# Performance work log

Measured on AMD Instinct MI355X. Metric: run time of the kernel, lower is better.

The kernel has to match this reference:

```python
import jax, jax.numpy as jnp
import numpy as np

B, S, D = 2, 2048, 2048
HQ, HKV = 16, 4
HD = D // HQ  # 128


def setup_inputs() -> dict:
    key = jax.random.key(0)
    ks = jax.random.split(key, 8)
    init = lambda k, sh: jax.random.normal(k, sh, dtype=jnp.float32) * 0.02
    return {
        "q": jax.random.normal(ks[0], (B, S, D), dtype=jnp.float32),
        "kv": jax.random.normal(ks[1], (B, S, D), dtype=jnp.float32),
        "attn_bias": jax.random.normal(ks[2], (1, HQ, 1, S), dtype=jnp.float32),
        "attention_mask": jnp.ones((B, S), dtype=bool),
        "Wq_w": init(ks[3], (D, D)), "Wq_b": jnp.zeros((D,), jnp.float32),
        "Wk_w": init(ks[4], (HKV * HD, D)), "Wk_b": jnp.zeros((HKV * HD,), jnp.float32),
        "Wv_w": init(ks[5], (HKV * HD, D)), "Wv_b": jnp.zeros((HKV * HD,), jnp.float32),
        "Wo_w": init(ks[6], (D, D)), "Wo_b": jnp.zeros((D,), jnp.float32),
    }


def reference(q, kv, attn_bias, attention_mask, Wq_w, Wq_b, Wk_w, Wk_b, Wv_w, Wv_b, Wo_w, Wo_b):
    # Projections (torch nn.Linear: y = x @ W.T + b)
    query = q @ Wq_w.T + Wq_b        # [B,S,D]
    key_ = kv @ Wk_w.T + Wk_b        # [B,S,HKV*HD]
    value = kv @ Wv_w.T + Wv_b       # [B,S,HKV*HD]

    qh = query.reshape(B, S, HQ, HD).transpose(0, 2, 1, 3)   # [B,HQ,S,HD]
    kh = key_.reshape(B, S, HKV, HD).transpose(0, 2, 1, 3)   # [B,HKV,S,HD]
    vh = value.reshape(B, S, HKV, HD).transpose(0, 2, 1, 3)

    # GQA repeat_kv == torch.repeat_interleave along head dim
    n_rep = HQ // HKV
    kh = jnp.repeat(kh, n_rep, axis=1)  # [B,HQ,S,HD]
    vh = jnp.repeat(vh, n_rep, axis=1)

    scale = 1.0 / np.sqrt(HD).astype(np.float32)
    scores = jnp.einsum('bhqd,bhkd->bhqk', qh, kh) * scale  # [B,HQ,S,S]
    scores = scores + attn_bias  # broadcast [1,HQ,1,S]

    min_val = jnp.finfo(scores.dtype).min
    # key padding mask (True = keep)
    scores = jnp.where(attention_mask[:, None, None, :], scores, min_val)
    # causal mask
    causal = jnp.tril(jnp.ones((S, S), dtype=bool))
    scores = jnp.where(causal[None, None, :, :], scores, min_val)

    attn = jax.nn.softmax(scores, axis=-1)
    out = jnp.einsum('bhqk,bhkd->bhqd', attn, vh)           # [B,HQ,S,HD]
    out = out.transpose(0, 2, 1, 3).reshape(B, S, D)
    return out @ Wo_w.T + Wo_b
```

## Files before the change

kernel.cpp:

```cpp
#include <hip/hip_runtime.h>

typedef __bf16 bf16_t;
typedef __bf16 bf16x8 __attribute__((ext_vector_type(8)));
typedef float  f32x4  __attribute__((ext_vector_type(4)));

#define B_SZ    2
#define S_LEN   2048
#define D_MODEL 2048
#define HQ_     16
#define HD_     128
#define KV_D    512

typedef __attribute__((address_space(1))) const unsigned int gas_u32;
typedef __attribute__((address_space(3))) unsigned int las_u32;
__device__ __forceinline__ void glds16(const void* g, void* l) {
    __builtin_amdgcn_global_load_lds((gas_u32*)g, (las_u32*)l, 16, 0, 0);
}

template<int CTRL>
__device__ __forceinline__ float dppf(float x) {
    return __builtin_bit_cast(float,
        __builtin_amdgcn_update_dpp(0, __builtin_bit_cast(int, x), CTRL, 0xF, 0xF, false));
}
__device__ __forceinline__ float redmax16(float x) {
    x = fmaxf(x, dppf<0xB1>(x));
    x = fmaxf(x, dppf<0x4E>(x));
    x = fmaxf(x, dppf<0x141>(x));
    x = fmaxf(x, dppf<0x140>(x));
    return x;
}
__device__ __forceinline__ float redsum16(float x) {
    x += dppf<0xB1>(x);
    x += dppf<0x4E>(x);
    x += dppf<0x141>(x);
    x += dppf<0x140>(x);
    return x;
}

#define CB0 2097152u
#define CB1 4194304u
#define CB2 5242880u
#define CB3 5505024u
#define CB4 5767168u
#define CB5 6815744u
__global__ __launch_bounds__(256) void cast_all(const float* s0, const float* s1, const float* s2,
                                                const float* s3, const float* s4, const float* s5,
                                                bf16_t* d0, bf16_t* d1, bf16_t* d2,
                                                bf16_t* d3, bf16_t* d4, bf16_t* d5) {
    unsigned g = blockIdx.x * 256 + threadIdx.x;
    const float* src; bf16_t* dst; unsigned off;
    if (g < CB2) {
        if (g < CB0)      { src = s0; dst = d0; off = 0; }
        else if (g < CB1) { src = s1; dst = d1; off = CB0; }
        else              { src = s2; dst = d2; off = CB1; }
    } else {
        if (g < CB3)      { src = s3; dst = d3; off = CB2; }
        else if (g < CB4) { src = s4; dst = d4; off = CB3; }
        else              { src = s5; dst = d5; off = CB4; }
    }
    unsigned i = g - off;
    float4 v = ((const float4*)src)[i];
    bf16_t tmp[4] = {(bf16_t)v.x, (bf16_t)v.y, (bf16_t)v.z, (bf16_t)v.w};
    ((ushort4*)dst)[i] = *(ushort4*)tmp;
}

template<bool OUT_BF16>
__device__ __forceinline__ void gemm_nt_body(bf16_t* As, bf16_t* Bs,
                                             const bf16_t* __restrict__ A,
                                             const bf16_t* __restrict__ Bm,
                                             const float* __restrict__ bias,
                                             void* __restrict__ C,
                                             int M, int N, int K, int bx, int by) {
    const int tid  = threadIdx.x;
    const int lane = tid & 63;
    const int w    = tid >> 6;
    const int l16  = lane & 15;
    const int quad = lane >> 4;
    const int m0   = by * 128;
    const int n0   = bx * 128;
    const int moff = (w & 1) * 64;
    const int noff = (w >> 1) * 64;

    const int srow = w * 32 + (lane >> 2);
    const int scol = ((lane & 3) ^ ((lane >> 3) & 3)) * 8;
    const bf16_t* Ar = A  + (size_t)(m0 + srow) * K + scol;
    const bf16_t* Br = Bm + (size_t)(n0 + srow) * K + scol;
    bf16_t* asw = As + w * 1024;
    bf16_t* bsw = Bs + w * 1024;

    f32x4 acc[4][4];
    for (int i = 0; i < 4; ++i)
        for (int j = 0; j < 4; ++j) acc[i][j] = (f32x4){0.f, 0.f, 0.f, 0.f};

    const int nkt = K >> 5;
    for (int kt = 0; kt < nkt; ++kt) {
        const int ko = kt * 32;
        __syncthreads();
        glds16(Ar + ko,                  asw);
        glds16(Ar + (size_t)16 * K + ko, asw + 512);
        glds16(Br + ko,                  bsw);
        glds16(Br + (size_t)16 * K + ko, bsw + 512);
        __syncthreads();

        bf16x8 af[4], bfr[4];
        for (int i = 0; i < 4; ++i) {
            int row = moff + i * 16 + l16;
            af[i] = *(const bf16x8*)&As[row * 32 + ((quad ^ (row >> 1)) & 3) * 8];
        }
        for (int j = 0; j < 4; ++j) {
            int row = noff + j * 16 + l16;
            bfr[j] = *(const bf16x8*)&Bs[row * 32 + ((quad ^ (row >> 1)) & 3) * 8];
        }
        for (int i = 0; i < 4; ++i)
            for (int j = 0; j < 4; ++j)
                acc[i][j] = __builtin_amdgcn_mfma_f32_16x16x32_bf16(af[i], bfr[j], acc[i][j], 0, 0, 0);
    }

    for (int i = 0; i < 4; ++i) {
        int row = m0 + moff + i * 16 + quad * 4;
        for (int j = 0; j < 4; ++j) {
            int col = n0 + noff + j * 16 + l16;
            float bv = bias[col];
            for (int r = 0; r < 4; ++r) {
                float v = acc[i][j][r] + bv;
                if (OUT_BF16) ((bf16_t*)C)[(size_t)(row + r) * N + col] = (bf16_t)v;
                else          ((float*)C)[(size_t)(row + r) * N + col] = v;
            }
        }
    }
}

template<bool OUT_BF16>
__global__ __launch_bounds__(256) void gemm_nt_bias(const bf16_t* __restrict__ A,
                                                    const bf16_t* __restrict__ Bm,
                                                    const float* __restrict__ bias,
                                                    void* __restrict__ C,
                                                    int M, int N, int K) {
    __shared__ bf16_t As[128 * 32];
    __shared__ bf16_t Bs[128 * 32];
    gemm_nt_body<OUT_BF16>(As, Bs, A, Bm, bias, C, M, N, K, blockIdx.x, blockIdx.y);
}

__global__ __launch_bounds__(256) void gemm_nt_bias_kv(const bf16_t* __restrict__ A,
                                                       const bf16_t* __restrict__ Bk,
                                                       const bf16_t* __restrict__ Bv,
                                                       const float* __restrict__ bk,
                                                       const float* __restrict__ bv,
                                                       bf16_t* __restrict__ Ck,
                                                       bf16_t* __restrict__ Cv,
                                                       int M, int N, int K) {
    __shared__ bf16_t As[128 * 32];
    __shared__ bf16_t Bs[128 * 32];
    if (blockIdx.z == 0)
        gemm_nt_body<true>(As, Bs, A, Bk, bk, Ck, M, N, K, blockIdx.x, blockIdx.y);
    else
        gemm_nt_body<true>(As, Bs, A, Bv, bv, Cv, M, N, K, blockIdx.x, blockIdx.y);
}

__global__ __launch_bounds__(256) void transpose_v(const bf16_t* __restrict__ src,
                                                   bf16_t* __restrict__ dst) {
    __shared__ bf16_t T[64 * 72];
    const int t  = threadIdx.x;
    const int s0 = blockIdx.x * 64, c0 = blockIdx.y * 64, b = blockIdx.z;
    const int r = t >> 3, c8 = (t & 7) * 8;
    const bf16_t* sp = src + ((size_t)b * S_LEN + s0) * KV_D + c0;
    for (int i = 0; i < 64; i += 32) {
        int s = r + i;
        *(uint4*)&T[s * 72 + (c8 ^ (((s >> 3) & 7) * 8))] =
            *(const uint4*)&sp[(size_t)s * KV_D + c8];
    }
    __syncthreads();
    const int dr = t >> 3, s8 = (t & 7) * 8;
    bf16_t* dp = dst + ((size_t)b * KV_D + c0) * S_LEN + s0;
    for (int i = 0; i < 64; i += 32) {
        int d = dr + i;
        bf16_t tmp[8];
        for (int j = 0; j < 8; ++j) {
            int s = s8 + j;
            tmp[j] = T[s * 72 + (((d & ~7) ^ (((s >> 3) & 7) * 8)) | (d & 7))];
        }
        *(uint4*)&dp[(size_t)d * S_LEN + s8] = *(uint4*)tmp;
    }
}

__device__ __forceinline__ int ks_addr(int r, int c) {
    int ch = c >> 3;
    return r * 128 + ((ch & 8) | ((ch ^ r) & 7)) * 8 + (c & 7);
}
__device__ __forceinline__ int vt_addr(int d, int k) {
    return d * 64 + (((k >> 3) ^ d) & 7) * 8 + (k & 7);
}
__device__ __forceinline__ int ps_addr(int row, int c) {
    int ph = (row ^ (row >> 1)) & 7;
    return row * 64 + (((c >> 3) ^ ph) & 7) * 8 + (c & 7);
}

struct Strip {
    float m[4];
    float l[4];
    f32x4 o[8];
};

__device__ __forceinline__ void score_softmax(f32x4* s, Strip& st, bool diag,
                                              int qbase, int k0, const float* Bls,
                                              bf16_t* psw, int l16, int quad) {
    const float SCL2E = 0.08838834764831845f * 1.44269504088896f;
    float rowmax[4];
    for (int r = 0; r < 4; ++r) rowmax[r] = -__builtin_inff();
    for (int n = 0; n < 4; ++n) {
        int kc = k0 + n * 16 + l16;
        float bv = Bls[kc];
        for (int r = 0; r < 4; ++r) {
            float v = fmaf(s[n][r], SCL2E, bv);
            if (diag && kc > qbase + quad * 4 + r) v = -__builtin_inff();
            s[n][r] = v;
            rowmax[r] = fmaxf(rowmax[r], v);
        }
    }
    float alpha[4], rowsum[4];
    for (int r = 0; r < 4; ++r) {
        float mx = redmax16(rowmax[r]);
        float mnew = fmaxf(st.m[r], mx);
        alpha[r] = exp2f(st.m[r] - mnew);
        st.m[r] = mnew;
        rowsum[r] = 0.f;
    }
    for (int n = 0; n < 4; ++n)
        for (int r = 0; r < 4; ++r) {
            float pv = exp2f(s[n][r] - st.m[r]);
            psw[ps_addr(quad * 4 + r, n * 16 + l16)] = (bf16_t)pv;
            rowsum[r] += pv;
        }
    for (int r = 0; r < 4; ++r) {
        rowsum[r] = redsum16(rowsum[r]);
        st.l[r] = st.l[r] * alpha[r] + rowsum[r];
    }
    for (int d = 0; d < 8; ++d)
        for (int r = 0; r < 4; ++r) st.o[d][r] *= alpha[r];
}

__global__ __launch_bounds__(256, 2) void flash_attn(const bf16_t* __restrict__ Qg,
                                                     const bf16_t* __restrict__ Kg,
                                                     const bf16_t* __restrict__ Vt,
                                                     const float* __restrict__ bias,
                                                     bf16_t* __restrict__ Og) {
    const int p   = blockIdx.x;
    const int h   = blockIdx.y;
    const int b   = blockIdx.z;
    const int qtL = p, qtH = 31 - p;
    const int q0L = qtL * 64, q0H = qtH * 64;
    const int kvh = h >> 2;

    __shared__ bf16_t Ks[64 * 128];
    __shared__ bf16_t Vts[128 * 64];
    __shared__ bf16_t Ps[4 * 2 * 1024];
    __shared__ float  Bls[S_LEN];

    const int tid  = threadIdx.x;
    const int lane = tid & 63;
    const int w    = tid >> 6;
    const int l16  = lane & 15;
    const int quad = lane >> 4;
    const float L2E = 1.44269504088896f;

    for (int i = 0; i < 2; ++i) {
        int idx = tid + i * 256;
        float4 v = ((const float4*)(bias + h * S_LEN))[idx];
        ((float4*)Bls)[idx] = make_float4(v.x * L2E, v.y * L2E, v.z * L2E, v.w * L2E);
    }

    const bf16_t* qrowL = Qg + (size_t)(b * S_LEN + q0L + w * 16 + l16) * D_MODEL + h * HD_;
    const bf16_t* qrowH = Qg + (size_t)(b * S_LEN + q0H + w * 16 + l16) * D_MODEL + h * HD_;
    bf16x8 qfL[4], qfH[4];
    for (int d = 0; d < 4; ++d) {
        qfL[d] = *(const bf16x8*)&qrowL[d * 32 + quad * 8];
        qfH[d] = *(const bf16x8*)&qrowH[d * 32 + quad * 8];
    }

    const int kr  = tid >> 2;
    const int kc4 = (tid & 3) * 4;
    const int vd  = tid >> 1;
    const int vc4 = (tid & 1) * 4;
    const bf16_t* kbase = Kg + (size_t)(b * S_LEN) * KV_D + kvh * HD_;
    const bf16_t* vbase = Vt + ((size_t)(b * 4 + kvh) * HD_ + vd) * S_LEN;
    uint4 kpre[4], vpre[4];
    auto prefetch = [&](int k0) {
        const bf16_t* kp = kbase + (size_t)(k0 + kr) * KV_D;
        for (int i = 0; i < 4; ++i) kpre[i] = *(const uint4*)&kp[(kc4 + i) * 8];
        const bf16_t* vp = vbase + k0;
        for (int i = 0; i < 4; ++i) vpre[i] = *(const uint4*)&vp[(vc4 + i) * 8];
    };
    prefetch(0);

    Strip sL, sH;
    for (int r = 0; r < 4; ++r) {
        sL.m[r] = -__builtin_inff(); sL.l[r] = 0.f;
        sH.m[r] = -__builtin_inff(); sH.l[r] = 0.f;
    }
    for (int d = 0; d < 8; ++d) {
        sL.o[d] = (f32x4){0.f, 0.f, 0.f, 0.f};
        sH.o[d] = (f32x4){0.f, 0.f, 0.f, 0.f};
    }

    bf16_t* pswH = &Ps[w * 2048];
    bf16_t* pswL = pswH + 1024;

    for (int kt = 0; kt <= qtH; ++kt) {
        const int k0 = kt * 64;
        __syncthreads();
        for (int i = 0; i < 4; ++i) *(uint4*)&Ks[ks_addr(kr, (kc4 + i) * 8)] = kpre[i];
        for (int i = 0; i < 4; ++i) *(uint4*)&Vts[vt_addr(vd, (vc4 + i) * 8)] = vpre[i];
        __syncthreads();
        if (kt < qtH) prefetch(k0 + 64);

        const bool doL = (kt <= qtL);

        f32x4 accH[4], accL[4];
        for (int n = 0; n < 4; ++n) {
            accH[n] = (f32x4){0.f, 0.f, 0.f, 0.f};
            accL[n] = (f32x4){0.f, 0.f, 0.f, 0.f};
        }
        for (int dstep = 0; dstep < 4; ++dstep)
            for (int n = 0; n < 4; ++n) {
                bf16x8 bb = *(const bf16x8*)&Ks[ks_addr(n * 16 + l16, dstep * 32 + quad * 8)];
                accH[n] = __builtin_amdgcn_mfma_f32_16x16x32_bf16(qfH[dstep], bb, accH[n], 0, 0, 0);
                if (doL)
                    accL[n] = __builtin_amdgcn_mfma_f32_16x16x32_bf16(qfL[dstep], bb, accL[n], 0, 0, 0);
            }

        score_softmax(accH, sH, kt == qtH, q0H + w * 16, k0, Bls, pswH, l16, quad);
        if (doL) score_softmax(accL, sL, kt == qtL, q0L + w * 16, k0, Bls, pswL, l16, quad);

        for (int kstep = 0; kstep < 2; ++kstep) {
            bf16x8 aH = *(const bf16x8*)&pswH[ps_addr(l16, kstep * 32 + quad * 8)];
            bf16x8 aL;
            if (doL) aL = *(const bf16x8*)&pswL[ps_addr(l16, kstep * 32 + quad * 8)];
            for (int d = 0; d < 8; ++d) {
                bf16x8 bb = *(const bf16x8*)&Vts[vt_addr(d * 16 + l16, kstep * 32 + quad * 8)];
                sH.o[d] = __builtin_amdgcn_mfma_f32_16x16x32_bf16(aH, bb, sH.o[d], 0, 0, 0);
                if (doL)
                    sL.o[d] = __builtin_amdgcn_mfma_f32_16x16x32_bf16(aL, bb, sL.o[d], 0, 0, 0);
            }
        }
    }

    auto write_out = [&](Strip& st, int q0) {
        bf16_t* dst = Og + (size_t)(b * S_LEN + q0 + w * 16) * D_MODEL + h * HD_;
        float inv[4];
        for (int r = 0; r < 4; ++r) inv[r] = __builtin_amdgcn_rcpf(st.l[r]);
        for (int d = 0; d < 8; ++d)
            for (int r = 0; r < 4; ++r) {
                float v = st.o[d][r] * inv[r];
                dst[(size_t)(quad * 4 + r) * D_MODEL + d * 16 + l16] = (bf16_t)v;
            }
    };
    write_out(sH, q0H);
    write_out(sL, q0L);
}

extern "C" void kernel_launch(void* const* d_in, const int* in_sizes, int n_in,
                              void* d_out, int out_size, void* d_ws, size_t ws_size,
                              hipStream_t stream) {
    const float* q         = (const float*)d_in[0];
    const float* kv        = (const float*)d_in[1];
    const float* attn_bias = (const float*)d_in[2];
    const float* Wq_w = (const float*)d_in[4];
    const float* Wq_b = (const float*)d_in[5];
    const float* Wk_w = (const float*)d_in[6];
    const float* Wk_b = (const float*)d_in[7];
    const float* Wv_w = (const float*)d_in[8];
    const float* Wv_b = (const float*)d_in[9];
    const float* Wo_w = (const float*)d_in[10];
    const float* Wo_b = (const float*)d_in[11];
    float* out = (float*)d_out;

    const size_t MROWS = (size_t)B_SZ * S_LEN;
    char* ws = (char*)d_ws;
    size_t off = 0;
    auto alloc = [&](size_t elems) { bf16_t* p = (bf16_t*)(ws + off); off += elems * sizeof(bf16_t); return p; };
    bf16_t* qb     = alloc(MROWS * D_MODEL);
    bf16_t* kvb    = alloc(MROWS * D_MODEL);
    bf16_t* Wqb    = alloc((size_t)D_MODEL * D_MODEL);
    bf16_t* Wkb    = alloc((size_t)KV_D * D_MODEL);
    bf16_t* Wvb    = alloc((size_t)KV_D * D_MODEL);
    bf16_t* Wob    = alloc((size_t)D_MODEL * D_MODEL);
    bf16_t* queryb = alloc(MROWS * D_MODEL);
    bf16_t* keyb   = alloc(MROWS * KV_D);
    bf16_t* valueb = alloc(MROWS * KV_D);
    bf16_t* vtb    = alloc(MROWS * KV_D);
    bf16_t* attnb  = alloc(MROWS * D_MODEL);
    (void)ws_size; (void)in_sizes; (void)n_in; (void)out_size;

    cast_all<<<dim3(CB5 / 256), dim3(256), 0, stream>>>(
        q, kv, Wq_w, Wk_w, Wv_w, Wo_w, qb, kvb, Wqb, Wkb, Wvb, Wob);

    gemm_nt_bias<true><<<dim3(D_MODEL / 128, MROWS / 128), dim3(256), 0, stream>>>(
        qb, Wqb, Wq_b, queryb, (int)MROWS, D_MODEL, D_MODEL);
    gemm_nt_bias_kv<<<dim3(KV_D / 128, MROWS / 128, 2), dim3(256), 0, stream>>>(
        kvb, Wkb, Wvb, Wk_b, Wv_b, keyb, valueb, (int)MROWS, KV_D, D_MODEL);

    transpose_v<<<dim3(S_LEN / 64, KV_D / 64, B_SZ), dim3(256), 0, stream>>>(valueb, vtb);

    flash_attn<<<dim3(16, HQ_, B_SZ), dim3(256), 0, stream>>>(
        queryb, keyb, vtb, attn_bias, attnb);

    gemm_nt_bias<false><<<dim3(D_MODEL / 128, MROWS / 128), dim3(256), 0, stream>>>(
        attnb, Wob, Wo_b, out, (int)MROWS, D_MODEL, D_MODEL);
}
```

Before: 467.4 us.

## Load K/V MFMA operands directly from global memory instead of LDS staging

Removes the shared-memory K and V tiles and the register prefetch that fed them. Each wave now loads its MFMA B operands straight from global memory (through the L1/L2 caches), and the two block syncs per KV tile become a single barrier. The smaller LDS footprint lets launch bounds go from 2 to 3 blocks per CU. In exchange, each of the four waves re-reads the same K/V data from cache, the loads are only partly coalesced, and the software prefetch that hid load latency is gone.

```diff
diff --git a/kernel.cpp b/kernel.cpp
--- a/kernel.cpp
+++ b/kernel.cpp
@@ -183,13 +183,6 @@
     }
 }
 
-__device__ __forceinline__ int ks_addr(int r, int c) {
-    int ch = c >> 3;
-    return r * 128 + ((ch & 8) | ((ch ^ r) & 7)) * 8 + (c & 7);
-}
-__device__ __forceinline__ int vt_addr(int d, int k) {
-    return d * 64 + (((k >> 3) ^ d) & 7) * 8 + (k & 7);
-}
 __device__ __forceinline__ int ps_addr(int row, int c) {
     int ph = (row ^ (row >> 1)) & 7;
     return row * 64 + (((c >> 3) ^ ph) & 7) * 8 + (c & 7);
@@ -239,7 +232,7 @@
         for (int r = 0; r < 4; ++r) st.o[d][r] *= alpha[r];
 }
 
-__global__ __launch_bounds__(256, 2) void flash_attn(const bf16_t* __restrict__ Qg,
+__global__ __launch_bounds__(256, 3) void flash_attn(const bf16_t* __restrict__ Qg,
                                                      const bf16_t* __restrict__ Kg,
                                                      const bf16_t* __restrict__ Vt,
                                                      const float* __restrict__ bias,
@@ -251,8 +244,6 @@
     const int q0L = qtL * 64, q0H = qtH * 64;
     const int kvh = h >> 2;
 
-    __shared__ bf16_t Ks[64 * 128];
-    __shared__ bf16_t Vts[128 * 64];
     __shared__ bf16_t Ps[4 * 2 * 1024];
     __shared__ float  Bls[S_LEN];
 
@@ -268,6 +259,7 @@
         float4 v = ((const float4*)(bias + h * S_LEN))[idx];
         ((float4*)Bls)[idx] = make_float4(v.x * L2E, v.y * L2E, v.z * L2E, v.w * L2E);
     }
+    __syncthreads();
 
     const bf16_t* qrowL = Qg + (size_t)(b * S_LEN + q0L + w * 16 + l16) * D_MODEL + h * HD_;
     const bf16_t* qrowH = Qg + (size_t)(b * S_LEN + q0H + w * 16 + l16) * D_MODEL + h * HD_;
@@ -277,20 +269,8 @@
         qfH[d] = *(const bf16x8*)&qrowH[d * 32 + quad * 8];
     }
 
-    const int kr  = tid >> 2;
-    const int kc4 = (tid & 3) * 4;
-    const int vd  = tid >> 1;
-    const int vc4 = (tid & 1) * 4;
-    const bf16_t* kbase = Kg + (size_t)(b * S_LEN) * KV_D + kvh * HD_;
-    const bf16_t* vbase = Vt + ((size_t)(b * 4 + kvh) * HD_ + vd) * S_LEN;
-    uint4 kpre[4], vpre[4];
-    auto prefetch = [&](int k0) {
-        const bf16_t* kp = kbase + (size_t)(k0 + kr) * KV_D;
-        for (int i = 0; i < 4; ++i) kpre[i] = *(const uint4*)&kp[(kc4 + i) * 8];
-        const bf16_t* vp = vbase + k0;
-        for (int i = 0; i < 4; ++i) vpre[i] = *(const uint4*)&vp[(vc4 + i) * 8];
-    };
-    prefetch(0);
+    const bf16_t* kln = Kg + ((size_t)(b * S_LEN + l16)) * KV_D + kvh * HD_ + quad * 8;
+    const bf16_t* vln = Vt + ((size_t)((b * 4 + kvh) * HD_ + l16)) * S_LEN + quad * 8;
 
     Strip sL, sH;
     for (int r = 0; r < 4; ++r) {
@@ -307,12 +287,7 @@
 
     for (int kt = 0; kt <= qtH; ++kt) {
         const int k0 = kt * 64;
-        __syncthreads();
-        for (int i = 0; i < 4; ++i) *(uint4*)&Ks[ks_addr(kr, (kc4 + i) * 8)] = kpre[i];
-        for (int i = 0; i < 4; ++i) *(uint4*)&Vts[vt_addr(vd, (vc4 + i) * 8)] = vpre[i];
-        __syncthreads();
-        if (kt < qtH) prefetch(k0 + 64);
-
+        __builtin_amdgcn_s_barrier();
         const bool doL = (kt <= qtL);
 
         f32x4 accH[4], accL[4];
@@ -320,13 +295,18 @@
             accH[n] = (f32x4){0.f, 0.f, 0.f, 0.f};
             accL[n] = (f32x4){0.f, 0.f, 0.f, 0.f};
         }
-        for (int dstep = 0; dstep < 4; ++dstep)
+        for (int dstep = 0; dstep < 4; ++dstep) {
+            bf16x8 kb[4];
+#pragma unroll
+            for (int n = 0; n < 4; ++n)
+                kb[n] = *(const bf16x8*)&kln[(size_t)(k0 + n * 16) * KV_D + dstep * 32];
+#pragma unroll
             for (int n = 0; n < 4; ++n) {
-                bf16x8 bb = *(const bf16x8*)&Ks[ks_addr(n * 16 + l16, dstep * 32 + quad * 8)];
-                accH[n] = __builtin_amdgcn_mfma_f32_16x16x32_bf16(qfH[dstep], bb, accH[n], 0, 0, 0);
+                accH[n] = __builtin_amdgcn_mfma_f32_16x16x32_bf16(qfH[dstep], kb[n], accH[n], 0, 0, 0);
                 if (doL)
-                    accL[n] = __builtin_amdgcn_mfma_f32_16x16x32_bf16(qfL[dstep], bb, accL[n], 0, 0, 0);
+                    accL[n] = __builtin_amdgcn_mfma_f32_16x16x32_bf16(qfL[dstep], kb[n], accL[n], 0, 0, 0);
             }
+        }
 
         score_softmax(accH, sH, kt == qtH, q0H + w * 16, k0, Bls, pswH, l16, quad);
         if (doL) score_softmax(accL, sL, kt == qtL, q0L + w * 16, k0, Bls, pswL, l16, quad);
@@ -335,11 +315,12 @@
             bf16x8 aH = *(const bf16x8*)&pswH[ps_addr(l16, kstep * 32 + quad * 8)];
             bf16x8 aL;
             if (doL) aL = *(const bf16x8*)&pswL[ps_addr(l16, kstep * 32 + quad * 8)];
+#pragma unroll
             for (int d = 0; d < 8; ++d) {
-                bf16x8 bb = *(const bf16x8*)&Vts[vt_addr(d * 16 + l16, kstep * 32 + quad * 8)];
-                sH.o[d] = __builtin_amdgcn_mfma_f32_16x16x32_bf16(aH, bb, sH.o[d], 0, 0, 0);
+                bf16x8 vb = *(const bf16x8*)&vln[(size_t)(d * 16) * S_LEN + k0 + kstep * 32];
+                sH.o[d] = __builtin_amdgcn_mfma_f32_16x16x32_bf16(aH, vb, sH.o[d], 0, 0, 0);
                 if (doL)
-                    sL.o[d] = __builtin_amdgcn_mfma_f32_16x16x32_bf16(aL, bb, sL.o[d], 0, 0, 0);
+                    sL.o[d] = __builtin_amdgcn_mfma_f32_16x16x32_bf16(aL, vb, sL.o[d], 0, 0, 0);
             }
         }
     }
```

After: 805.8 us. 72.4% more time.
